# Kernel tuning notes

Measured on AMD Instinct MI355X. Metric: run time of the kernel, lower is better.

The kernel has to match this reference:

```python
import jax, jax.numpy as jnp
import numpy as np

B = 4096
D_IN = 1024
D_H = 1024


def setup_inputs() -> dict:
    key = jax.random.key(0)
    ks = jax.random.split(key, 6)
    s_h = 1.0 / np.sqrt(D_H)
    return {
        "x": jax.random.normal(ks[0], (B, D_IN), dtype=jnp.float32),
        "h": jax.random.normal(ks[1], (B, D_H), dtype=jnp.float32),
        "c": jax.random.normal(ks[2], (B, D_H), dtype=jnp.float32),
        # hidden_lin: Linear(D_H, 4*D_H) with bias; stored as [in, out] for x @ W
        "W_h": jax.random.uniform(ks[3], (D_H, 4 * D_H), jnp.float32, -s_h, s_h),
        "b_h": jax.random.uniform(ks[4], (4 * D_H,), jnp.float32, -s_h, s_h),
        # input_lin: Linear(D_IN, 4*D_H, bias=False)
        "W_x": jax.random.uniform(ks[5], (D_IN, 4 * D_H), jnp.float32, -s_h, s_h),
    }


def reference(x, h, c, W_h, b_h, W_x):
    # ifgo = hidden_lin(h) + input_lin(x)  -> [B, 4H]
    ifgo = h @ W_h + b_h + x @ W_x
    i, f, g, o = jnp.split(ifgo, 4, axis=-1)
    c_next = jax.nn.sigmoid(f) * c + jax.nn.sigmoid(i) * jnp.tanh(g)
    h_next = jax.nn.sigmoid(o) * jnp.tanh(c_next)
    return (h_next, c_next)
```

## Files before the change

kernel.cpp:

```cpp
#include <hip/hip_runtime.h>


#define BM 128
#define BK 32
#define KTILES 64

typedef __attribute__((ext_vector_type(8))) short bf16x8;
typedef __attribute__((ext_vector_type(8))) short short8;
typedef __attribute__((ext_vector_type(4))) short s16x4;
typedef __attribute__((ext_vector_type(4))) float f32x4;

__device__ __forceinline__ unsigned short f2bf(float f) {
  unsigned int u = __builtin_bit_cast(unsigned int, f);
  u += 0x7fffu + ((u >> 16) & 1u);
  return (unsigned short)(u >> 16);
}
__device__ __forceinline__ float bf2f(unsigned short s) {
  return __builtin_bit_cast(float, ((unsigned int)s) << 16);
}
__device__ __forceinline__ float sigm(float v) { return 1.0f / (1.0f + __expf(-v)); }
__device__ __forceinline__ float tanh_f(float v) {
  float e = __expf(2.0f * v);
  return 1.0f - 2.0f / (e + 1.0f);
}

#define GLOAD_LDS16(gsrc, ldst)                                      \
  __builtin_amdgcn_global_load_lds(                                  \
      (const __attribute__((address_space(1))) void*)(gsrc),         \
      (__attribute__((address_space(3))) void*)(ldst), 16, 0, 0)


__global__ void __launch_bounds__(256) convA_kernel(
    const float* __restrict__ x, const float* __restrict__ h,
    short* __restrict__ PAhi, short* __restrict__ PAlo) {
  int t = blockIdx.x * 256 + threadIdx.x;
  int lp = t & 63;
  int rg = (t >> 6) & 255;
  int kt = t >> 14;
  int row = rg * 16 + (lp & 15);
  int k = kt * 32 + (lp >> 4) * 8;
  const float* src = (k < 1024) ? (h + row * 1024 + k) : (x + row * 1024 + (k - 1024));
  float v[8];
  *reinterpret_cast<f32x4*>(v) = *reinterpret_cast<const f32x4*>(src);
  *reinterpret_cast<f32x4*>(v + 4) = *reinterpret_cast<const f32x4*>(src + 4);
  short8 hi, lo;
#pragma unroll
  for (int j = 0; j < 8; ++j) {
    unsigned short hb = f2bf(v[j]);
    hi[j] = (short)hb;
    lo[j] = (short)f2bf(v[j] - bf2f(hb));
  }
  *reinterpret_cast<short8*>(PAhi + (size_t)t * 8) = hi;
  *reinterpret_cast<short8*>(PAlo + (size_t)t * 8) = lo;
}

__global__ void __launch_bounds__(256) convW_kernel(
    const float* __restrict__ Wh, const float* __restrict__ Wx,
    short* __restrict__ PWhi, short* __restrict__ PWlo) {
  int t = blockIdx.x * 256 + threadIdx.x;
  int lp = t & 63;
  int ng = (t >> 6) & 255;
  int kt = t >> 14;
  int n = ng * 16 + (lp & 15);
  int k = kt * 32 + (lp >> 4) * 8;
  const float* src = (k < 1024) ? (Wh + (size_t)k * 4096 + n)
                                : (Wx + (size_t)(k - 1024) * 4096 + n);
  float v[8];
#pragma unroll
  for (int e = 0; e < 8; ++e) v[e] = src[(size_t)e * 4096];
  short8 hi, lo;
#pragma unroll
  for (int j = 0; j < 8; ++j) {
    unsigned short hb = f2bf(v[j]);
    hi[j] = (short)hb;
    lo[j] = (short)f2bf(v[j] - bf2f(hb));
  }
  *reinterpret_cast<short8*>(PWhi + (size_t)t * 8) = hi;
  *reinterpret_cast<short8*>(PWlo + (size_t)t * 8) = lo;
}

__global__ void __launch_bounds__(256, 2) lstm_gemm_kernel(
    const short* __restrict__ PAhi, const short* __restrict__ PAlo,
    const short* __restrict__ PWhi, const short* __restrict__ PWlo,
    const float* __restrict__ c, const float* __restrict__ bh,
    float* __restrict__ out) {
  __shared__ __align__(16) char lds[2][32768];

  const int tid = threadIdx.x;
  const int lane = tid & 63;
  const int wave = tid >> 6;
  const int wm = wave >> 1;
  const int wn = wave & 1;

  const int bid = blockIdx.x;
  const int mt = bid & 31;
  const int nt = bid >> 5;
  const int b0 = mt * BM;
  const int j0 = nt * 32;

  const short* srcbase = (wave == 0) ? PAhi
                       : (wave == 1) ? PAlo
                       : (wave == 2) ? PWhi : PWlo;
  const int ab0 = b0 >> 4;
  const int nt2 = nt * 2;

  auto stage = [&](int kt, int buf) {
#pragma unroll
    for (int i = 0; i < 8; ++i) {
      int grp = (wave < 2) ? (ab0 + i) : ((i >> 1) * 64 + nt2 + (i & 1));
      const short* src = srcbase + ((size_t)(kt * 256 + grp) * 512) + lane * 8;
      char* dst = &lds[buf][(wave * 8 + i) * 1024];
      GLOAD_LDS16(src, dst);
    }
  };

  const int fc = lane & 15;
  f32x4 acc[4][4];
#pragma unroll
  for (int g = 0; g < 4; ++g) {
    float bv = bh[g * 1024 + j0 + wn * 16 + fc];
    f32x4 b4 = {bv, bv, bv, bv};
#pragma unroll
    for (int m = 0; m < 4; ++m) acc[m][g] = b4;
  }

  stage(0, 0);
  __syncthreads();
  int cur = 0;

#pragma unroll 1
  for (int kt = 0; kt < KTILES; ++kt) {
    if (kt + 1 < KTILES) stage(kt + 1, cur ^ 1);

    const char* bp = lds[cur];
    bf16x8 ah[4], al[4], whf[4], wlf[4];
#pragma unroll
    for (int m = 0; m < 4; ++m) {
      ah[m] = *reinterpret_cast<const bf16x8*>(bp + (wm * 4 + m) * 1024 + lane * 16);
      al[m] = *reinterpret_cast<const bf16x8*>(bp + 8192 + (wm * 4 + m) * 1024 + lane * 16);
    }
#pragma unroll
    for (int g = 0; g < 4; ++g) {
      whf[g] = *reinterpret_cast<const bf16x8*>(bp + 16384 + (g * 2 + wn) * 1024 + lane * 16);
      wlf[g] = *reinterpret_cast<const bf16x8*>(bp + 24576 + (g * 2 + wn) * 1024 + lane * 16);
    }

#pragma unroll
    for (int m = 0; m < 4; ++m)
#pragma unroll
      for (int g = 0; g < 4; ++g) {
        acc[m][g] = __builtin_amdgcn_mfma_f32_16x16x32_bf16(ah[m], whf[g], acc[m][g], 0, 0, 0);
        acc[m][g] = __builtin_amdgcn_mfma_f32_16x16x32_bf16(al[m], whf[g], acc[m][g], 0, 0, 0);
        acc[m][g] = __builtin_amdgcn_mfma_f32_16x16x32_bf16(ah[m], wlf[g], acc[m][g], 0, 0, 0);
      }
    __syncthreads();
    cur ^= 1;
  }

  const int gcol = j0 + wn * 16 + fc;
  const int fr4 = (lane >> 4) * 4;
#pragma unroll
  for (int m = 0; m < 4; ++m) {
    int grow_base = b0 + wm * 64 + m * 16 + fr4;
#pragma unroll
    for (int r = 0; r < 4; ++r) {
      int grow = grow_base + r;
      float iv = acc[m][0][r];
      float fv = acc[m][1][r];
      float gv = acc[m][2][r];
      float ov = acc[m][3][r];
      float cold = c[grow * 1024 + gcol];
      float cn = sigm(fv) * cold + sigm(iv) * tanh_f(gv);
      float hn = sigm(ov) * tanh_f(cn);
      out[grow * 1024 + gcol] = hn;
      out[4096 * 1024 + grow * 1024 + gcol] = cn;
    }
  }
}

__global__ void __launch_bounds__(256, 2) lstm_cell_kernel(
    const float* __restrict__ x, const float* __restrict__ h,
    const float* __restrict__ c, const float* __restrict__ Wh,
    const float* __restrict__ bh, const float* __restrict__ Wx,
    float* __restrict__ out) {
  __shared__ __align__(16) unsigned short Ahi[BM][40];
  __shared__ __align__(16) unsigned short Alo[BM][40];
  __shared__ __align__(16) unsigned short Whi_s[4][32][40];
  __shared__ __align__(16) unsigned short Wlo_s[4][32][40];

  const int tid = threadIdx.x;
  const int lane = tid & 63;
  const int wave = tid >> 6;
  const int wm = wave >> 1;
  const int wn = wave & 1;
  const int bid = blockIdx.x;
  const int mt = bid & 31;
  const int nt = bid >> 5;
  const int b0 = mt * BM;
  const int j0 = nt * 32;
  const int a_c = tid & 7;
  const int a_r0 = tid >> 3;
  const int w_gt = tid >> 6;
  const int w_n = tid & 31;
  const int w_kh = (tid >> 5) & 1;
  const int w_col = w_gt * 1024 + j0 + w_n;
  const int fc = lane & 15;
  const int k0 = (lane >> 4) * 8;

  f32x4 acc[4][4];
#pragma unroll
  for (int g = 0; g < 4; ++g) {
    float bv = bh[g * 1024 + j0 + wn * 16 + fc];
    f32x4 b4 = {bv, bv, bv, bv};
#pragma unroll
    for (int m = 0; m < 4; ++m) acc[m][g] = b4;
  }
  f32x4 av[4];
  float wv[16];
  auto load_tiles = [&](int kt, f32x4* avp, float* wvp) {
    const float* As = (kt < 32) ? h : x;
    const float* Ws = (kt < 32) ? Wh : Wx;
    const int krow = (kt & 31) * BK;
#pragma unroll
    for (int p = 0; p < 4; ++p) {
      int r = a_r0 + p * 32;
      avp[p] = *reinterpret_cast<const f32x4*>(As + (b0 + r) * 1024 + krow + a_c * 4);
    }
#pragma unroll
    for (int e = 0; e < 16; ++e) wvp[e] = Ws[(krow + w_kh * 16 + e) * 4096 + w_col];
  };
  load_tiles(0, av, wv);
#pragma unroll 1
  for (int kt = 0; kt < KTILES; ++kt) {
#pragma unroll
    for (int p = 0; p < 4; ++p) {
      int r = a_r0 + p * 32;
      s16x4 hi, lo;
#pragma unroll
      for (int j = 0; j < 4; ++j) {
        float f = av[p][j];
        unsigned short hb = f2bf(f);
        hi[j] = (short)hb;
        lo[j] = (short)f2bf(f - bf2f(hb));
      }
      *reinterpret_cast<s16x4*>(&Ahi[r][a_c * 4]) = hi;
      *reinterpret_cast<s16x4*>(&Alo[r][a_c * 4]) = lo;
    }
#pragma unroll
    for (int q0 = 0; q0 < 4; ++q0) {
      int q = (q0 + (w_n >> 3)) & 3;
      s16x4 hi, lo;
#pragma unroll
      for (int j = 0; j < 4; ++j) {
        float f = wv[q * 4 + j];
        unsigned short hb = f2bf(f);
        hi[j] = (short)hb;
        lo[j] = (short)f2bf(f - bf2f(hb));
      }
      *reinterpret_cast<s16x4*>(&Whi_s[w_gt][w_n][w_kh * 16 + q * 4]) = hi;
      *reinterpret_cast<s16x4*>(&Wlo_s[w_gt][w_n][w_kh * 16 + q * 4]) = lo;
    }
    __syncthreads();
    bf16x8 ah[4], al[4], bhf[4], blf[4];
#pragma unroll
    for (int m = 0; m < 4; ++m) {
      int rr = wm * 64 + m * 16 + fc;
      ah[m] = *reinterpret_cast<const bf16x8*>(&Ahi[rr][k0]);
      al[m] = *reinterpret_cast<const bf16x8*>(&Alo[rr][k0]);
    }
    const int nn = wn * 16 + fc;
#pragma unroll
    for (int g = 0; g < 4; ++g) {
      bhf[g] = *reinterpret_cast<const bf16x8*>(&Whi_s[g][nn][k0]);
      blf[g] = *reinterpret_cast<const bf16x8*>(&Wlo_s[g][nn][k0]);
    }
    if (kt + 1 < KTILES) load_tiles(kt + 1, av, wv);
#pragma unroll
    for (int m = 0; m < 4; ++m)
#pragma unroll
      for (int g = 0; g < 4; ++g) {
        acc[m][g] = __builtin_amdgcn_mfma_f32_16x16x32_bf16(ah[m], bhf[g], acc[m][g], 0, 0, 0);
        acc[m][g] = __builtin_amdgcn_mfma_f32_16x16x32_bf16(al[m], bhf[g], acc[m][g], 0, 0, 0);
        acc[m][g] = __builtin_amdgcn_mfma_f32_16x16x32_bf16(ah[m], blf[g], acc[m][g], 0, 0, 0);
      }
    __syncthreads();
  }
  const int gcol = j0 + wn * 16 + fc;
  const int fr4 = (lane >> 4) * 4;
#pragma unroll
  for (int m = 0; m < 4; ++m) {
    int grow_base = b0 + wm * 64 + m * 16 + fr4;
#pragma unroll
    for (int r = 0; r < 4; ++r) {
      int grow = grow_base + r;
      float iv = acc[m][0][r];
      float fv = acc[m][1][r];
      float gv = acc[m][2][r];
      float ov = acc[m][3][r];
      float cold = c[grow * 1024 + gcol];
      float cn = sigm(fv) * cold + sigm(iv) * tanh_f(gv);
      float hn = sigm(ov) * tanh_f(cn);
      out[grow * 1024 + gcol] = hn;
      out[4096 * 1024 + grow * 1024 + gcol] = cn;
    }
  }
}

extern "C" void kernel_launch(void* const* d_in, const int* in_sizes, int n_in,
                              void* d_out, int out_size, void* d_ws,
                              size_t ws_size, hipStream_t stream) {
  (void)in_sizes; (void)n_in; (void)out_size;
  const float* x = (const float*)d_in[0];
  const float* h = (const float*)d_in[1];
  const float* c = (const float*)d_in[2];
  const float* Wh = (const float*)d_in[3];
  const float* bh = (const float*)d_in[4];
  const float* Wx = (const float*)d_in[5];
  float* out = (float*)d_out;

  const size_t QUAD = (size_t)8 * 1024 * 1024;
  if (ws_size >= 4 * QUAD * sizeof(short)) {
    short* PAhi = (short*)d_ws;
    short* PAlo = PAhi + QUAD;
    short* PWhi = PAlo + QUAD;
    short* PWlo = PWhi + QUAD;
    convA_kernel<<<dim3(4096), dim3(256), 0, stream>>>(x, h, PAhi, PAlo);
    convW_kernel<<<dim3(4096), dim3(256), 0, stream>>>(Wh, Wx, PWhi, PWlo);
    lstm_gemm_kernel<<<dim3(1024), dim3(256), 0, stream>>>(PAhi, PAlo, PWhi,
                                                           PWlo, c, bh, out);
  } else {
    lstm_cell_kernel<<<dim3(1024), dim3(256), 0, stream>>>(x, h, c, Wh, bh, Wx,
                                                           out);
  }
}
```

Measured before the change: 296.2 us.

## Stage input and weight conversion through LDS for coalesced global reads

The fp32-to-split-bf16 conversion kernels now load contiguous row chunks of x/h and of W_h/W_x into shared memory with 16-byte vector loads, then transpose/repack from LDS into the packed MFMA fragment layout. The old convW did strided scalar loads (stride 4096 floats) and convA did per-lane 32-byte loads, so global read coalescing was poor. Grid sizes shrink so each block handles a larger tile, at the cost of LDS traffic, a barrier, and possible LDS bank conflicts on the column reads.

After: 282.8 us. 4.5% less time.

```diff
diff --git a/kernel.cpp b/kernel.cpp
--- a/kernel.cpp
+++ b/kernel.cpp
@@ -33,50 +33,93 @@
 __global__ void __launch_bounds__(256) convA_kernel(
     const float* __restrict__ x, const float* __restrict__ h,
     short* __restrict__ PAhi, short* __restrict__ PAlo) {
-  int t = blockIdx.x * 256 + threadIdx.x;
-  int lp = t & 63;
-  int rg = (t >> 6) & 255;
-  int kt = t >> 14;
-  int row = rg * 16 + (lp & 15);
-  int k = kt * 32 + (lp >> 4) * 8;
-  const float* src = (k < 1024) ? (h + row * 1024 + k) : (x + row * 1024 + (k - 1024));
-  float v[8];
-  *reinterpret_cast<f32x4*>(v) = *reinterpret_cast<const f32x4*>(src);
-  *reinterpret_cast<f32x4*>(v + 4) = *reinterpret_cast<const f32x4*>(src + 4);
-  short8 hi, lo;
-#pragma unroll
-  for (int j = 0; j < 8; ++j) {
-    unsigned short hb = f2bf(v[j]);
-    hi[j] = (short)hb;
-    lo[j] = (short)f2bf(v[j] - bf2f(hb));
-  }
-  *reinterpret_cast<short8*>(PAhi + (size_t)t * 8) = hi;
-  *reinterpret_cast<short8*>(PAlo + (size_t)t * 8) = lo;
+  __shared__ __align__(16) float At[16][268];
+  const int bid = blockIdx.x;
+  const int rg = bid >> 3;
+  const int ks = bid & 7;
+  const int t = threadIdx.x;
+
+  {
+    const int rr = t >> 4;
+    const int cc = t & 15;
+    const int row = rg * 16 + rr;
+    const int kbase = ks * 256;
+    const float* srcrow = (kbase < 1024) ? (h + (size_t)row * 1024 + kbase)
+                                         : (x + (size_t)row * 1024 + (kbase - 1024));
+#pragma unroll
+    for (int j = 0; j < 4; ++j) {
+      *reinterpret_cast<f32x4*>(&At[rr][j * 64 + cc * 4]) =
+          *reinterpret_cast<const f32x4*>(srcrow + j * 64 + cc * 4);
+    }
+  }
+  __syncthreads();
+
+  const int kt_l = t >> 5;
+  const int l0 = t & 31;
+  const int kt = ks * 8 + kt_l;
+  const size_t base = (size_t)(kt * 256 + rg) * 512;
+#pragma unroll
+  for (int half = 0; half < 2; ++half) {
+    const int l = l0 + half * 32;
+    const int fc = l & 15;
+    const int kq = l >> 4;
+    short8 hi, lo;
+#pragma unroll
+    for (int e = 0; e < 8; ++e) {
+      float f = At[fc][kt_l * 32 + kq * 8 + e];
+      unsigned short hb = f2bf(f);
+      hi[e] = (short)hb;
+      lo[e] = (short)f2bf(f - bf2f(hb));
+    }
+    *reinterpret_cast<short8*>(PAhi + base + l * 8) = hi;
+    *reinterpret_cast<short8*>(PAlo + base + l * 8) = lo;
+  }
 }
 
 __global__ void __launch_bounds__(256) convW_kernel(
     const float* __restrict__ Wh, const float* __restrict__ Wx,
     short* __restrict__ PWhi, short* __restrict__ PWlo) {
-  int t = blockIdx.x * 256 + threadIdx.x;
-  int lp = t & 63;
-  int ng = (t >> 6) & 255;
-  int kt = t >> 14;
-  int n = ng * 16 + (lp & 15);
-  int k = kt * 32 + (lp >> 4) * 8;
-  const float* src = (k < 1024) ? (Wh + (size_t)k * 4096 + n)
-                                : (Wx + (size_t)(k - 1024) * 4096 + n);
-  float v[8];
-#pragma unroll
-  for (int e = 0; e < 8; ++e) v[e] = src[(size_t)e * 4096];
-  short8 hi, lo;
-#pragma unroll
-  for (int j = 0; j < 8; ++j) {
-    unsigned short hb = f2bf(v[j]);
-    hi[j] = (short)hb;
-    lo[j] = (short)f2bf(v[j] - bf2f(hb));
-  }
-  *reinterpret_cast<short8*>(PWhi + (size_t)t * 8) = hi;
-  *reinterpret_cast<short8*>(PWlo + (size_t)t * 8) = lo;
+  __shared__ __align__(16) float Wt[32][268];
+  const int bid = blockIdx.x;
+  const int kb = bid >> 4;
+  const int ns = bid & 15;
+  const int t = threadIdx.x;
+
+  {
+    const int rr = t >> 3;
+    const int cc = t & 7;
+    const int kg = kb * 32 + rr;
+    const float* srcrow = (kb < 32) ? (Wh + (size_t)kg * 4096)
+                                    : (Wx + (size_t)(kg - 1024 / 32 * 32 + rr - rr) * 4096 + (size_t)(kg - 1024) * 0);
+    srcrow = (kg < 1024) ? (Wh + (size_t)kg * 4096)
+                         : (Wx + (size_t)(kg - 1024) * 4096);
+#pragma unroll
+    for (int j = 0; j < 8; ++j) {
+      const int n = ns * 256 + j * 32 + cc * 4;
+      *reinterpret_cast<f32x4*>(&Wt[rr][j * 32 + cc * 4]) =
+          *reinterpret_cast<const f32x4*>(srcrow + n);
+    }
+  }
+  __syncthreads();
+
+  const int fc = t & 15;
+  const int grp_l = t >> 4;
+  const int nl = t;
+  const size_t grp = (size_t)ns * 16 + grp_l;
+  const size_t base = ((size_t)kb * 256 + grp) * 512;
+#pragma unroll
+  for (int kq = 0; kq < 4; ++kq) {
+    short8 hi, lo;
+#pragma unroll
+    for (int e = 0; e < 8; ++e) {
+      float f = Wt[kq * 8 + e][nl];
+      unsigned short hb = f2bf(f);
+      hi[e] = (short)hb;
+      lo[e] = (short)f2bf(f - bf2f(hb));
+    }
+    *reinterpret_cast<short8*>(PWhi + base + (kq * 16 + fc) * 8) = hi;
+    *reinterpret_cast<short8*>(PWlo + base + (kq * 16 + fc) * 8) = lo;
+  }
 }
 
 __global__ void __launch_bounds__(256, 2) lstm_gemm_kernel(
@@ -324,8 +367,8 @@
     short* PAlo = PAhi + QUAD;
     short* PWhi = PAlo + QUAD;
     short* PWlo = PWhi + QUAD;
-    convA_kernel<<<dim3(4096), dim3(256), 0, stream>>>(x, h, PAhi, PAlo);
-    convW_kernel<<<dim3(4096), dim3(256), 0, stream>>>(Wh, Wx, PWhi, PWlo);
+    convA_kernel<<<dim3(2048), dim3(256), 0, stream>>>(x, h, PAhi, PAlo);
+    convW_kernel<<<dim3(1024), dim3(256), 0, stream>>>(Wh, Wx, PWhi, PWlo);
     lstm_gemm_kernel<<<dim3(1024), dim3(256), 0, stream>>>(PAhi, PAlo, PWhi,
                                                            PWlo, c, bh, out);
   } else {
```
